# Optimization experiments

Hardware: AMD Instinct MI355X
Metric: run time of the kernel (lower is better)

Reference implementation:

```python
import jax, jax.numpy as jnp
import numpy as np

N, F_IN, H, OUT = 8192, 512, 128, 3
DEG_P = 16.0 / N  # avg degree ~16


def setup_inputs() -> dict:
    key = jax.random.key(0)
    ks = jax.random.split(key, 10)
    x = jax.random.normal(ks[0], (N, F_IN), dtype=jnp.float32)
    adj = (jax.random.uniform(ks[1], (N, N)) < DEG_P).astype(jnp.float32)

    def glorot(k, shape):
        lim = float(np.sqrt(6.0 / (shape[0] + shape[1])))
        return jax.random.uniform(k, shape, jnp.float32, -lim, lim)

    return {
        "x": x,
        "adj": adj,
        "Wl1": glorot(ks[2], (F_IN, H)),   # neighbor-agg weight, layer 1
        "Wr1": glorot(ks[3], (F_IN, H)),   # root/self weight, layer 1
        "b1": jnp.zeros((H,), jnp.float32),
        "Wl2": glorot(ks[4], (H, H)),
        "Wr2": glorot(ks[5], (H, H)),
        "b2": jnp.zeros((H,), jnp.float32),
        "Wd": glorot(ks[6], (H, OUT)),
        "bd": jnp.zeros((OUT,), jnp.float32),
    }


def _sage(x, adj, Wl, Wr, b):
    # GraphSAGE-mean: mean over neighbors via dense adjacency, then transform.
    deg = jnp.maximum(adj.sum(axis=1, keepdims=True), 1.0)  # [N,1]
    agg = (adj @ x) / deg                                    # [N,F]
    return agg @ Wl + x @ Wr + b


def _cdist(y):
    # pairwise Euclidean distances, grad-safe sqrt (zero grad on zero dist)
    sq = jnp.sum(y * y, axis=-1)                             # [N]
    d2 = jnp.maximum(sq[:, None] + sq[None, :] - 2.0 * (y @ y.T), 0.0)
    return jnp.where(d2 > 0, jnp.sqrt(jnp.where(d2 > 0, d2, 1.0)), 0.0)


def reference(x, adj, Wl1, Wr1, b1, Wl2, Wr2, b2, Wd, bd):
    h = jax.nn.relu(_sage(x, adj, Wl1, Wr1, b1))
    # dropout p=0.5 is identity in eval mode
    h = _sage(h, adj, Wl2, Wr2, b2)
    y = h @ Wd + bd                                          # [N,3]
    return _cdist(y)                                         # [N,N]
```

## Files before the change

### kernel.cpp

```cpp
#include <hip/hip_runtime.h>
#include <math.h>

#define NN 8192
#define FIN 512
#define HD 128
#define CAP 128

typedef float f32x4 __attribute__((ext_vector_type(4)));

__global__ __launch_bounds__(256) void k_gemm(
    const float* __restrict__ x, const float* __restrict__ Wl1,
    const float* __restrict__ Wr1, const float* __restrict__ b1,
    const float* __restrict__ Wl2, const float* __restrict__ Wr2,
    const float* __restrict__ b2, const float* __restrict__ Wd,
    const float* __restrict__ bd,
    float* __restrict__ xl, float* __restrict__ xr,
    float4* __restrict__ wsm)
{
    __shared__ float As[32][32];
    __shared__ float Bs[32][128];
    const int tid = threadIdx.x;
    const int b = blockIdx.x;

    if (b == 512) {
        const int t = tid;
        if (t < HD) {
            float l0 = 0, l1 = 0, l2 = 0, r0 = 0, r1 = 0, r2 = 0;
            for (int c = 0; c < HD; ++c) {
                const float w0 = Wd[c * 3 + 0], w1 = Wd[c * 3 + 1], w2 = Wd[c * 3 + 2];
                const float wl = Wl2[t * HD + c];
                const float wr = Wr2[t * HD + c];
                l0 = fmaf(wl, w0, l0); l1 = fmaf(wl, w1, l1); l2 = fmaf(wl, w2, l2);
                r0 = fmaf(wr, w0, r0); r1 = fmaf(wr, w1, r1); r2 = fmaf(wr, w2, r2);
            }
            wsm[t]       = make_float4(l0, l1, l2, 0.f);
            wsm[128 + t] = make_float4(r0, r1, r2, 0.f);
            if (t == 0) {
                float c0 = bd[0], c1 = bd[1], c2 = bd[2];
                for (int c = 0; c < HD; ++c) {
                    c0 = fmaf(b2[c], Wd[c * 3 + 0], c0);
                    c1 = fmaf(b2[c], Wd[c * 3 + 1], c1);
                    c2 = fmaf(b2[c], Wd[c * 3 + 2], c2);
                }
                wsm[256] = make_float4(c0, c1, c2, 0.f);
            }
        }
        return;
    }

    const bool left = (b < 256);
    const float* W = left ? Wl1 : Wr1;
    float* Cout    = left ? xl  : xr;
    const int row0 = (b & 255) * 32;
    const int rg = tid >> 5, cg = tid & 31;
    const int ar = tid >> 3, ak = (tid & 7) * 4;
    const int bk = tid >> 5, bc = (tid & 31) * 4;
    float acc[4][4] = {};
    for (int ch = 0; ch < FIN / 32; ++ch) {
        const int kc = ch * 32;
        __syncthreads();
        const float4 va = *(const float4*)(x + (size_t)(row0 + ar) * FIN + kc + ak);
        As[ak + 0][ar] = va.x; As[ak + 1][ar] = va.y;
        As[ak + 2][ar] = va.z; As[ak + 3][ar] = va.w;
        #pragma unroll
        for (int it = 0; it < 4; ++it)
            *(float4*)&Bs[bk + 8 * it][bc] =
                *(const float4*)(W + (size_t)(kc + bk + 8 * it) * HD + bc);
        __syncthreads();
        #pragma unroll
        for (int k = 0; k < 32; ++k) {
            const float4 a4 = *(const float4*)&As[k][rg * 4];
            const float4 b4 = *(const float4*)&Bs[k][cg * 4];
            const float av[4] = {a4.x, a4.y, a4.z, a4.w};
            const float bv[4] = {b4.x, b4.y, b4.z, b4.w};
            #pragma unroll
            for (int a = 0; a < 4; ++a)
                #pragma unroll
                for (int bb = 0; bb < 4; ++bb)
                    acc[a][bb] = fmaf(av[a], bv[bb], acc[a][bb]);
        }
    }
    float4 bias = make_float4(0.f, 0.f, 0.f, 0.f);
    if (!left) bias = ((const float4*)b1)[cg];
    #pragma unroll
    for (int a = 0; a < 4; ++a)
        *(float4*)(Cout + (size_t)(row0 + rg * 4 + a) * HD + cg * 4) =
            make_float4(acc[a][0] + bias.x, acc[a][1] + bias.y,
                        acc[a][2] + bias.z, acc[a][3] + bias.w);
}

__global__ __launch_bounds__(256) void k_scanagg(
    const float* __restrict__ adj, const float* __restrict__ xl,
    const float* __restrict__ xrb, const float4* __restrict__ wsm,
    int* __restrict__ nbr, int* __restrict__ degi, float* __restrict__ degf,
    float4* __restrict__ u4, float4* __restrict__ v4)
{
    __shared__ int lists[4][CAP];
    const int w = threadIdx.x >> 6, lane = threadIdx.x & 63;
    const int i = blockIdx.x * 4 + w;
    int* lst = lists[w];

    const f32x4* row = (const f32x4*)(adj + (size_t)i * NN);
    const unsigned long long lmask = (1ull << lane) - 1ull;
    int cnt = 0;
    for (int it = 0; it < NN / 256; ++it) {
        const f32x4 a = __builtin_nontemporal_load(&row[it * 64 + lane]);
        const float vals[4] = {a.x, a.y, a.z, a.w};
        #pragma unroll
        for (int e = 0; e < 4; ++e) {
            const bool nz = (vals[e] != 0.0f);
            const unsigned long long m = __ballot(nz);
            if (nz) {
                const int p = cnt + (int)__popcll(m & lmask);
                if (p < CAP) lst[p] = (it * 64 + lane) * 4 + e;
            }
            cnt += (int)__popcll(m);
        }
    }
    const int d = cnt < CAP ? cnt : CAP;
    const float inv = 1.0f / fmaxf((float)cnt, 1.0f);
    if (lane < d)      nbr[(size_t)i * CAP + lane]      = lst[lane];
    if (lane + 64 < d) nbr[(size_t)i * CAP + lane + 64] = lst[lane + 64];
    if (lane == 0) { degi[i] = d; degf[i] = fmaxf((float)cnt, 1.0f); }

    const int half = lane >> 5;
    const int cl = lane & 31;
    f32x4 s = {0.f, 0.f, 0.f, 0.f};
    for (int t = 0; t < d; t += 8) {
        #pragma unroll
        for (int e = 0; e < 4; ++e) {
            const int idx = t + 2 * e + half;
            const bool ok = idx < d;
            const int j = ok ? lst[idx] : 0;
            const f32x4 a = ((const f32x4*)(xl + (size_t)j * HD))[cl];
            if (ok) s += a;
        }
    }
    s.x += __shfl_xor(s.x, 32);
    s.y += __shfl_xor(s.y, 32);
    s.z += __shfl_xor(s.z, 32);
    s.w += __shfl_xor(s.w, 32);

    const f32x4 rr = ((const f32x4*)(xrb + (size_t)i * HD))[cl];
    f32x4 h;
    h.x = fmaxf(fmaf(s.x, inv, rr.x), 0.f);
    h.y = fmaxf(fmaf(s.y, inv, rr.y), 0.f);
    h.z = fmaxf(fmaf(s.z, inv, rr.z), 0.f);
    h.w = fmaxf(fmaf(s.w, inv, rr.w), 0.f);

    const float4 w0 = wsm[cl * 4 + 0], w1 = wsm[cl * 4 + 1];
    const float4 w2 = wsm[cl * 4 + 2], w3 = wsm[cl * 4 + 3];
    const float4 q0 = wsm[128 + cl * 4 + 0], q1 = wsm[128 + cl * 4 + 1];
    const float4 q2 = wsm[128 + cl * 4 + 2], q3 = wsm[128 + cl * 4 + 3];
    float u0 = h.x * w0.x + h.y * w1.x + h.z * w2.x + h.w * w3.x;
    float u1 = h.x * w0.y + h.y * w1.y + h.z * w2.y + h.w * w3.y;
    float u2 = h.x * w0.z + h.y * w1.z + h.z * w2.z + h.w * w3.z;
    float v0 = h.x * q0.x + h.y * q1.x + h.z * q2.x + h.w * q3.x;
    float v1 = h.x * q0.y + h.y * q1.y + h.z * q2.y + h.w * q3.y;
    float v2 = h.x * q0.z + h.y * q1.z + h.z * q2.z + h.w * q3.z;
    #pragma unroll
    for (int off = 16; off; off >>= 1) {
        u0 += __shfl_xor(u0, off); u1 += __shfl_xor(u1, off); u2 += __shfl_xor(u2, off);
        v0 += __shfl_xor(v0, off); v1 += __shfl_xor(v1, off); v2 += __shfl_xor(v2, off);
    }
    if (lane == 0) {
        u4[i] = make_float4(u0, u1, u2, 0.f);
        v4[i] = make_float4(v0, v1, v2, 0.f);
    }
}

__global__ __launch_bounds__(256) void k_ycomb(
    const float4* __restrict__ u4, const float4* __restrict__ v4,
    const int* __restrict__ nbr, const int* __restrict__ degi,
    const float* __restrict__ degf, const float4* __restrict__ wsm,
    float4* __restrict__ y4)
{
    const int hw = threadIdx.x >> 5;
    const int lane = threadIdx.x & 31;
    const int i = blockIdx.x * 8 + hw;
    const int d = degi[i];
    const float inv = 1.0f / degf[i];
    const int* lst = nbr + (size_t)i * CAP;
    float s0 = 0.f, s1 = 0.f, s2 = 0.f;
    for (int base = 0; base + lane < d; base += 32) {
        const float4 u = u4[lst[base + lane]];
        s0 += u.x; s1 += u.y; s2 += u.z;
    }
    #pragma unroll
    for (int off = 16; off; off >>= 1) {
        s0 += __shfl_xor(s0, off); s1 += __shfl_xor(s1, off); s2 += __shfl_xor(s2, off);
    }
    if (lane == 0) {
        const float4 v = v4[i];
        const float4 c = wsm[256];
        y4[i] = make_float4(fmaf(s0, inv, v.x + c.x),
                            fmaf(s1, inv, v.y + c.y),
                            fmaf(s2, inv, v.z + c.z), 0.f);
    }
}

__global__ __launch_bounds__(256) void k_cdist(
    const float4* __restrict__ y4, float* __restrict__ out)
{
    __shared__ float4 yis[32];
    const int t = threadIdx.x;
    const int i0 = blockIdx.y * 32;
    if (t < 32) yis[t] = y4[i0 + t];
    __syncthreads();
    const int j0 = blockIdx.x * 1024 + t * 4;
    const float4 a0 = y4[j0 + 0], a1 = y4[j0 + 1];
    const float4 a2 = y4[j0 + 2], a3 = y4[j0 + 3];
    float* op = out + (size_t)i0 * NN + j0;
    #pragma unroll 4
    for (int ii = 0; ii < 32; ++ii) {
        const float4 yi = yis[ii];
        f32x4 r;
        { const float dx = yi.x - a0.x, dy = yi.y - a0.y, dz = yi.z - a0.z;
          r.x = sqrtf(fmaf(dx, dx, fmaf(dy, dy, dz * dz))); }
        { const float dx = yi.x - a1.x, dy = yi.y - a1.y, dz = yi.z - a1.z;
          r.y = sqrtf(fmaf(dx, dx, fmaf(dy, dy, dz * dz))); }
        { const float dx = yi.x - a2.x, dy = yi.y - a2.y, dz = yi.z - a2.z;
          r.z = sqrtf(fmaf(dx, dx, fmaf(dy, dy, dz * dz))); }
        { const float dx = yi.x - a3.x, dy = yi.y - a3.y, dz = yi.z - a3.z;
          r.w = sqrtf(fmaf(dx, dx, fmaf(dy, dy, dz * dz))); }
        __builtin_nontemporal_store(r, (f32x4*)op);
        op += NN;
    }
}

extern "C" void kernel_launch(void* const* d_in, const int* in_sizes, int n_in,
                              void* d_out, int out_size, void* d_ws, size_t ws_size,
                              hipStream_t stream) {
    const float* x   = (const float*)d_in[0];
    const float* adj = (const float*)d_in[1];
    const float* Wl1 = (const float*)d_in[2];
    const float* Wr1 = (const float*)d_in[3];
    const float* b1  = (const float*)d_in[4];
    const float* Wl2 = (const float*)d_in[5];
    const float* Wr2 = (const float*)d_in[6];
    const float* b2  = (const float*)d_in[7];
    const float* Wd  = (const float*)d_in[8];
    const float* bd  = (const float*)d_in[9];
    float* out = (float*)d_out;

    char* ws = (char*)d_ws;
    const size_t nbr_b  = (size_t)NN * CAP * 4;
    const size_t deg_b  = (size_t)NN * 4;
    const size_t vec_b  = (size_t)NN * 16;
    const size_t wsm_b  = 272 * 16;
    const size_t small_total = nbr_b + 2 * deg_b + 3 * vec_b + wsm_b;
    const size_t xl_b = (size_t)NN * HD * 4;

    size_t off = 0;
    int*    nbr  = (int*)(ws + off);    off += nbr_b;
    int*    degi = (int*)(ws + off);    off += deg_b;
    float*  degf = (float*)(ws + off);  off += deg_b;
    float4* u4   = (float4*)(ws + off); off += vec_b;
    float4* v4   = (float4*)(ws + off); off += vec_b;
    float4* y4   = (float4*)(ws + off); off += vec_b;
    float4* wsm  = (float4*)(ws + off); off += wsm_b;

    char* big = (ws_size >= small_total + 2 * xl_b) ? (ws + off) : (char*)d_out;
    float* xl  = (float*)(big);
    float* xrb = (float*)(big + xl_b);

    k_gemm<<<513, 256, 0, stream>>>(x, Wl1, Wr1, b1, Wl2, Wr2, b2, Wd, bd,
                                    xl, xrb, wsm);

    k_scanagg<<<NN / 4, 256, 0, stream>>>(adj, xl, xrb, wsm,
                                          nbr, degi, degf, u4, v4);

    k_ycomb<<<NN / 8, 256, 0, stream>>>(u4, v4, nbr, degi, degf, wsm, y4);

    k_cdist<<<dim3(NN / 1024, NN / 32), 256, 0, stream>>>(y4, out);
}
```

Before: 145.0 us.

## Fuse neighbor feature gather into adjacency scan loop

```diff
diff --git a/kernel.cpp b/kernel.cpp
--- a/kernel.cpp
+++ b/kernel.cpp
@@ -103,6 +103,7 @@
     const f32x4* row = (const f32x4*)(adj + (size_t)i * NN);
     const unsigned long long lmask = (1ull << lane) - 1ull;
     int cnt = 0;
+    float s0 = 0.f, s1 = 0.f;
     for (int it = 0; it < NN / 256; ++it) {
         const f32x4 a = __builtin_nontemporal_load(&row[it * 64 + lane]);
         const float vals[4] = {a.x, a.y, a.z, a.w};
@@ -115,6 +116,14 @@
                 if (p < CAP) lst[p] = (it * 64 + lane) * 4 + e;
             }
             cnt += (int)__popcll(m);
+            unsigned long long mm = m;
+            while (mm) {
+                const int bit = (int)__builtin_ctzll(mm);
+                mm &= mm - 1;
+                const int j = (it * 64 + bit) * 4 + e;
+                const float2 g = ((const float2*)(xl + (size_t)j * HD))[lane];
+                s0 += g.x; s1 += g.y;
+            }
         }
     }
     const int d = cnt < CAP ? cnt : CAP;
@@ -123,43 +132,19 @@
     if (lane + 64 < d) nbr[(size_t)i * CAP + lane + 64] = lst[lane + 64];
     if (lane == 0) { degi[i] = d; degf[i] = fmaxf((float)cnt, 1.0f); }
 
-    const int half = lane >> 5;
-    const int cl = lane & 31;
-    f32x4 s = {0.f, 0.f, 0.f, 0.f};
-    for (int t = 0; t < d; t += 8) {
-        #pragma unroll
-        for (int e = 0; e < 4; ++e) {
-            const int idx = t + 2 * e + half;
-            const bool ok = idx < d;
-            const int j = ok ? lst[idx] : 0;
-            const f32x4 a = ((const f32x4*)(xl + (size_t)j * HD))[cl];
-            if (ok) s += a;
-        }
-    }
-    s.x += __shfl_xor(s.x, 32);
-    s.y += __shfl_xor(s.y, 32);
-    s.z += __shfl_xor(s.z, 32);
-    s.w += __shfl_xor(s.w, 32);
-
-    const f32x4 rr = ((const f32x4*)(xrb + (size_t)i * HD))[cl];
-    f32x4 h;
-    h.x = fmaxf(fmaf(s.x, inv, rr.x), 0.f);
-    h.y = fmaxf(fmaf(s.y, inv, rr.y), 0.f);
-    h.z = fmaxf(fmaf(s.z, inv, rr.z), 0.f);
-    h.w = fmaxf(fmaf(s.w, inv, rr.w), 0.f);
-
-    const float4 w0 = wsm[cl * 4 + 0], w1 = wsm[cl * 4 + 1];
-    const float4 w2 = wsm[cl * 4 + 2], w3 = wsm[cl * 4 + 3];
-    const float4 q0 = wsm[128 + cl * 4 + 0], q1 = wsm[128 + cl * 4 + 1];
-    const float4 q2 = wsm[128 + cl * 4 + 2], q3 = wsm[128 + cl * 4 + 3];
-    float u0 = h.x * w0.x + h.y * w1.x + h.z * w2.x + h.w * w3.x;
-    float u1 = h.x * w0.y + h.y * w1.y + h.z * w2.y + h.w * w3.y;
-    float u2 = h.x * w0.z + h.y * w1.z + h.z * w2.z + h.w * w3.z;
-    float v0 = h.x * q0.x + h.y * q1.x + h.z * q2.x + h.w * q3.x;
-    float v1 = h.x * q0.y + h.y * q1.y + h.z * q2.y + h.w * q3.y;
-    float v2 = h.x * q0.z + h.y * q1.z + h.z * q2.z + h.w * q3.z;
+    const float2 rr = ((const float2*)(xrb + (size_t)i * HD))[lane];
+    const float h0 = fmaxf(fmaf(s0, inv, rr.x), 0.f);
+    const float h1 = fmaxf(fmaf(s1, inv, rr.y), 0.f);
+    const float4 w0 = wsm[2 * lane], w1 = wsm[2 * lane + 1];
+    const float4 q0 = wsm[128 + 2 * lane], q1 = wsm[128 + 2 * lane + 1];
+    float u0 = h0 * w0.x + h1 * w1.x;
+    float u1 = h0 * w0.y + h1 * w1.y;
+    float u2 = h0 * w0.z + h1 * w1.z;
+    float v0 = h0 * q0.x + h1 * q1.x;
+    float v1 = h0 * q0.y + h1 * q1.y;
+    float v2 = h0 * q0.z + h1 * q1.z;
     #pragma unroll
-    for (int off = 16; off; off >>= 1) {
+    for (int off = 32; off; off >>= 1) {
         u0 += __shfl_xor(u0, off); u1 += __shfl_xor(u1, off); u2 += __shfl_xor(u2, off);
         v0 += __shfl_xor(v0, off); v1 += __shfl_xor(v1, off); v2 += __shfl_xor(v2, off);
     }
```

New measurement: 143.7 us. Within noise of the previous version (-0.8%).
